# Kernel optimization log

Measured on AMD Instinct MI355X. Metric: run time of the kernel, lower is better.

Reference implementation:

```python
import jax, jax.numpy as jnp
import numpy as np

H = 10  # hidden_dim

def _lstm_layer(x_tbd, w_ih, w_hh, b_ih, b_hh):
    # x_tbd: [T, B, D]; w_ih: [4H, D]; w_hh: [4H, H]; biases [4H]
    B = x_tbd.shape[1]
    h0 = jnp.zeros((B, H), x_tbd.dtype)
    c0 = jnp.zeros((B, H), x_tbd.dtype)
    # precompute input projections for all timesteps: [T, B, 4H]
    xg = jnp.einsum('tbd,gd->tbg', x_tbd, w_ih) + b_ih + b_hh

    def step(carry, xg_t):
        h, c = carry
        gates = xg_t + h @ w_hh.T  # [B, 4H]
        i, f, g, o = jnp.split(gates, 4, axis=-1)  # torch gate order i,f,g,o
        i = jax.nn.sigmoid(i); f = jax.nn.sigmoid(f)
        g = jnp.tanh(g); o = jax.nn.sigmoid(o)
        c = f * c + i * g
        h = o * jnp.tanh(c)
        return (h, c), h

    (hT, cT), hs = jax.lax.scan(step, (h0, c0), xg)
    return hs, hT  # hs: [T, B, H]

def setup_inputs() -> dict:
    key = jax.random.key(0)
    ks = jax.random.split(key, 11)
    B, T, D = 32768, 28, 28
    s0 = 1.0 / np.sqrt(H)
    u = lambda k, shape: jax.random.uniform(k, shape, jnp.float32, -s0, s0)
    return {
        'x': jax.random.normal(ks[0], (B, T, D), jnp.float32),
        'w_ih0': u(ks[1], (4 * H, D)),
        'w_hh0': u(ks[2], (4 * H, H)),
        'b_ih0': u(ks[3], (4 * H,)),
        'b_hh0': u(ks[4], (4 * H,)),
        'w_ih1': u(ks[5], (4 * H, H)),
        'w_hh1': u(ks[6], (4 * H, H)),
        'b_ih1': u(ks[7], (4 * H,)),
        'b_hh1': u(ks[8], (4 * H,)),
        'w_cls': u(ks[9], (10, H)),
        'b_cls': u(ks[10], (10,)),
    }

def reference(x, w_ih0, w_hh0, b_ih0, b_hh0, w_ih1, w_hh1, b_ih1, b_hh1, w_cls, b_cls):
    x_tbd = jnp.swapaxes(x, 0, 1)  # [T, B, D]
    hs0, _ = _lstm_layer(x_tbd, w_ih0, w_hh0, b_ih0, b_hh0)
    _, hT1 = _lstm_layer(hs0, w_ih1, w_hh1, b_ih1, b_hh1)  # hT1 = h_n[-1]
    return hT1 @ w_cls.T + b_cls  # [B, 10]
```

## Files before the change

### kernel.cpp

```cpp
#include <hip/hip_runtime.h>


#define HDIM 10
#define DDIM 28
#define TSTEPS 28

typedef __attribute__((ext_vector_type(8))) short short8;
typedef __attribute__((ext_vector_type(4))) float f32x4;

__device__ __forceinline__ unsigned short bf16_rne(float f) {
    unsigned u = __builtin_bit_cast(unsigned, f);
    u += 0x7FFFu + ((u >> 16) & 1u);
    return (unsigned short)(u >> 16);
}
__device__ __forceinline__ float bf16_f(unsigned short h) {
    unsigned u = ((unsigned)h) << 16;
    return __builtin_bit_cast(float, u);
}
__device__ __forceinline__ unsigned pk_hl(float v) {
    unsigned a, p;
    const float z = 0.0f;
    asm("v_cvt_pk_bf16_f32 %0, %1, %2" : "=v"(a) : "v"(v), "v"(z));
    const float hif = __builtin_bit_cast(float, a << 16);
    const float d = v - hif;
    asm("v_cvt_pk_bf16_f32 %0, %1, %2" : "=v"(p) : "v"(v), "v"(d));
    return p;
}
__device__ __forceinline__ float sig_f(float v) {
    return __builtin_amdgcn_rcpf(1.0f + __expf(-v));
}
__device__ __forceinline__ float tanh_f(float v) {
    return 2.0f * __builtin_amdgcn_rcpf(1.0f + __expf(-2.0f * v)) - 1.0f;
}

#define FENCE() __asm volatile("" ::: "memory")
#define WR32(arrp, sidx, val) (*(unsigned*)&(arrp)[(sidx)] = (val))

__global__ __launch_bounds__(64) void lstm2_mfma_kernel(
    const float* __restrict__ x,
    const float* __restrict__ w_ih0, const float* __restrict__ w_hh0,
    const float* __restrict__ b_ih0, const float* __restrict__ b_hh0,
    const float* __restrict__ w_ih1, const float* __restrict__ w_hh1,
    const float* __restrict__ b_ih1, const float* __restrict__ b_hh1,
    const float* __restrict__ w_cls, const float* __restrict__ b_cls,
    float* __restrict__ out)
{
    __shared__ unsigned short uA0[16 * 136];
    __shared__ unsigned short uA1[16 * 72];
    __shared__ float hfin[16 * 12];

    const int l  = threadIdx.x;
    const int lm = l & 15;
    const int q  = l >> 4;
    const int sbase = blockIdx.x * 16;

    for (int i = l; i < 16 * 22; i += 64) uA0[(i / 22) * 136 + 114 + (i % 22)] = 0;
    for (int i = l; i < 16 * 12; i += 64) uA1[(i / 12) * 72 + 60 + (i % 12)] = 0;

    short8 B0[4][4], B1[4][2];
    const bool gvalid = (lm < 10);
    #pragma unroll
    for (int T = 0; T < 4; ++T) {
        const int g = 10 * T + lm;
        #pragma unroll
        for (int c = 0; c < 4; ++c) {
            #pragma unroll
            for (int j = 0; j < 8; ++j) {
                const int kk = 32 * c + 8 * q + j;
                unsigned short bits = 0;
                if (gvalid && kk < 114) {
                    if (kk < 76) {
                        const int j2 = kk >> 1;
                        const float w = (j2 < 28) ? w_ih0[g * 28 + j2]
                                                  : w_hh0[g * 10 + (j2 - 28)];
                        bits = bf16_rne(w);
                    } else {
                        const int d = kk - 76;
                        const float w = (d < 28) ? w_ih0[g * 28 + d]
                                                 : w_hh0[g * 10 + (d - 28)];
                        const unsigned short hi = bf16_rne(w);
                        bits = bf16_rne(w - bf16_f(hi));
                    }
                }
                B0[T][c][j] = (short)bits;
            }
        }
        #pragma unroll
        for (int c = 0; c < 2; ++c) {
            #pragma unroll
            for (int j = 0; j < 8; ++j) {
                const int kk = 32 * c + 8 * q + j;
                unsigned short bits = 0;
                if (gvalid && kk < 60) {
                    if (kk < 40) {
                        const int j2 = kk >> 1;
                        const float w = (j2 < 10) ? w_ih1[g * 10 + j2]
                                                  : w_hh1[g * 10 + (j2 - 10)];
                        bits = bf16_rne(w);
                    } else {
                        const int d = kk - 40;
                        const float w = (d < 10) ? w_ih1[g * 10 + d]
                                                 : w_hh1[g * 10 + (d - 10)];
                        const unsigned short hi = bf16_rne(w);
                        bits = bf16_rne(w - bf16_f(hi));
                    }
                }
                B1[T][c][j] = (short)bits;
            }
        }
    }

    float bias0[4], bias1[4];
    #pragma unroll
    for (int T = 0; T < 4; ++T) {
        const int g = 10 * T + lm;
        bias0[T] = gvalid ? (b_ih0[g] + b_hh0[g]) : 0.0f;
        bias1[T] = gvalid ? (b_ih1[g] + b_hh1[g]) : 0.0f;
    }

    int xoff[7], lofsA[7], lofsB[7]; float xn[7];
    #pragma unroll
    for (int i = 0; i < 7; ++i) {
        const int f = l + 64 * i;
        const int sm = f / 28, d = f - 28 * sm;
        lofsA[i] = sm * 136 + 2 * d;
        lofsB[i] = sm * 136 + 76 + d;
        xoff[i] = (sbase + sm) * (TSTEPS * DDIM) + d;
        xn[i] = x[xoff[i]];
    }
    #pragma unroll
    for (int i = 0; i < 7; ++i) {
        const unsigned p = pk_hl(xn[i]);
        WR32(uA0, lofsA[i], p);
        uA0[lofsB[i]] = (unsigned short)p;
    }
    if (lm < 10) {
        #pragma unroll
        for (int r = 0; r < 4; ++r) {
            const int m = 4 * q + r;
            unsigned short* r0 = &uA0[m * 136];
            WR32(r0, 56 + 2 * lm, 0u); r0[104 + lm] = 0;
            unsigned short* r1 = &uA1[m * 72];
            WR32(r1, 2 * lm, 0u);      r1[40 + lm] = 0;
            WR32(r1, 20 + 2 * lm, 0u); r1[50 + lm] = 0;
        }
    }
    FENCE();

    float c0s[4] = {0, 0, 0, 0}, c1s[4] = {0, 0, 0, 0};
    float h1v[4] = {0, 0, 0, 0};
    float h0v[4];
    short8 A0f[4], A1f[2];

    #pragma unroll
    for (int c = 0; c < 4; ++c)
        A0f[c] = *(const short8*)&uA0[lm * 136 + 32 * c + 8 * q];
    FENCE();
    #pragma unroll
    for (int i = 0; i < 7; ++i) { xoff[i] += DDIM; xn[i] = x[xoff[i]]; }
    {
        f32x4 C[4];
        #pragma unroll
        for (int T = 0; T < 4; ++T) {
            f32x4 acc = {bias0[T], bias0[T], bias0[T], bias0[T]};
            #pragma unroll
            for (int c = 0; c < 4; ++c)
                acc = __builtin_amdgcn_mfma_f32_16x16x32_bf16(A0f[c], B0[T][c], acc, 0, 0, 0);
            C[T] = acc;
        }
        #pragma unroll
        for (int r = 0; r < 4; ++r) {
            const float i0 = sig_f(C[0][r]);
            const float f0 = sig_f(C[1][r]);
            const float g0 = tanh_f(C[2][r]);
            const float o0 = sig_f(C[3][r]);
            const float c0 = f0 * c0s[r] + i0 * g0;
            c0s[r] = c0;
            h0v[r] = o0 * tanh_f(c0);
        }
        if (lm < 10) {
            #pragma unroll
            for (int r = 0; r < 4; ++r) {
                const int m = 4 * q + r;
                const unsigned p0 = pk_hl(h0v[r]);
                unsigned short* r0 = &uA0[m * 136];
                WR32(r0, 56 + 2 * lm, p0); r0[104 + lm] = (unsigned short)p0;
                unsigned short* r1 = &uA1[m * 72];
                WR32(r1, 2 * lm, p0);      r1[40 + lm] = (unsigned short)p0;
            }
        }
        #pragma unroll
        for (int i = 0; i < 7; ++i) {
            const unsigned p = pk_hl(xn[i]);
            WR32(uA0, lofsA[i], p);
            uA0[lofsB[i]] = (unsigned short)p;
        }
    }
    FENCE();

    #pragma unroll 1
    for (int t = 0; t < TSTEPS - 1; ++t) {
        #pragma unroll
        for (int c = 0; c < 2; ++c)
            A1f[c] = *(const short8*)&uA1[lm * 72 + 32 * c + 8 * q];
        #pragma unroll
        for (int c = 0; c < 4; ++c)
            A0f[c] = *(const short8*)&uA0[lm * 136 + 32 * c + 8 * q];
        FENCE();

        if (t < TSTEPS - 2) {
            #pragma unroll
            for (int i = 0; i < 7; ++i) { xoff[i] += DDIM; xn[i] = x[xoff[i]]; }
        }

        f32x4 C[4], D[4];
        #pragma unroll
        for (int T = 0; T < 4; ++T) {
            f32x4 accD = {bias1[T], bias1[T], bias1[T], bias1[T]};
            #pragma unroll
            for (int c = 0; c < 2; ++c)
                accD = __builtin_amdgcn_mfma_f32_16x16x32_bf16(A1f[c], B1[T][c], accD, 0, 0, 0);
            D[T] = accD;
            f32x4 accC = {bias0[T], bias0[T], bias0[T], bias0[T]};
            #pragma unroll
            for (int c = 0; c < 4; ++c)
                accC = __builtin_amdgcn_mfma_f32_16x16x32_bf16(A0f[c], B0[T][c], accC, 0, 0, 0);
            C[T] = accC;
        }

        #pragma unroll
        for (int r = 0; r < 4; ++r) {
            const float i1 = sig_f(D[0][r]);
            const float f1 = sig_f(D[1][r]);
            const float g1 = tanh_f(D[2][r]);
            const float o1 = sig_f(D[3][r]);
            const float c1 = f1 * c1s[r] + i1 * g1;
            c1s[r] = c1;
            h1v[r] = o1 * tanh_f(c1);
            const float i0 = sig_f(C[0][r]);
            const float f0 = sig_f(C[1][r]);
            const float g0 = tanh_f(C[2][r]);
            const float o0 = sig_f(C[3][r]);
            const float c0 = f0 * c0s[r] + i0 * g0;
            c0s[r] = c0;
            h0v[r] = o0 * tanh_f(c0);
        }

        if (lm < 10) {
            #pragma unroll
            for (int r = 0; r < 4; ++r) {
                const int m = 4 * q + r;
                const unsigned p1 = pk_hl(h1v[r]);
                unsigned short* r1 = &uA1[m * 72];
                WR32(r1, 20 + 2 * lm, p1); r1[50 + lm] = (unsigned short)p1;
                const unsigned p0 = pk_hl(h0v[r]);
                WR32(r1, 2 * lm, p0);      r1[40 + lm] = (unsigned short)p0;
                unsigned short* r0 = &uA0[m * 136];
                WR32(r0, 56 + 2 * lm, p0); r0[104 + lm] = (unsigned short)p0;
            }
        }
        if (t < TSTEPS - 2) {
            #pragma unroll
            for (int i = 0; i < 7; ++i) {
                const unsigned p = pk_hl(xn[i]);
                WR32(uA0, lofsA[i], p);
                uA0[lofsB[i]] = (unsigned short)p;
            }
        }
        FENCE();
    }

    {
        #pragma unroll
        for (int c = 0; c < 2; ++c)
            A1f[c] = *(const short8*)&uA1[lm * 72 + 32 * c + 8 * q];
        FENCE();
        f32x4 D[4];
        #pragma unroll
        for (int T = 0; T < 4; ++T) {
            f32x4 acc = {bias1[T], bias1[T], bias1[T], bias1[T]};
            #pragma unroll
            for (int c = 0; c < 2; ++c)
                acc = __builtin_amdgcn_mfma_f32_16x16x32_bf16(A1f[c], B1[T][c], acc, 0, 0, 0);
            D[T] = acc;
        }
        #pragma unroll
        for (int r = 0; r < 4; ++r) {
            const float i1 = sig_f(D[0][r]);
            const float f1 = sig_f(D[1][r]);
            const float g1 = tanh_f(D[2][r]);
            const float o1 = sig_f(D[3][r]);
            const float c1 = f1 * c1s[r] + i1 * g1;
            h1v[r] = o1 * tanh_f(c1);
        }
    }

    if (lm < 10) {
        #pragma unroll
        for (int r = 0; r < 4; ++r) hfin[(4 * q + r) * 12 + lm] = h1v[r];
    }
    FENCE();
    if (lm < 10) {
        float wc[10];
        #pragma unroll
        for (int j = 0; j < 10; ++j) wc[j] = w_cls[lm * 10 + j];
        const float bo = b_cls[lm];
        #pragma unroll
        for (int r = 0; r < 4; ++r) {
            const int m = 4 * q + r;
            float acc = bo;
            #pragma unroll
            for (int j = 0; j < 10; ++j) acc += hfin[m * 12 + j] * wc[j];
            out[(size_t)(sbase + m) * 10 + lm] = acc;
        }
    }
}

extern "C" void kernel_launch(void* const* d_in, const int* in_sizes, int n_in,
                              void* d_out, int out_size, void* d_ws, size_t ws_size,
                              hipStream_t stream) {
    const float* x     = (const float*)d_in[0];
    const float* w_ih0 = (const float*)d_in[1];
    const float* w_hh0 = (const float*)d_in[2];
    const float* b_ih0 = (const float*)d_in[3];
    const float* b_hh0 = (const float*)d_in[4];
    const float* w_ih1 = (const float*)d_in[5];
    const float* w_hh1 = (const float*)d_in[6];
    const float* b_ih1 = (const float*)d_in[7];
    const float* b_hh1 = (const float*)d_in[8];
    const float* w_cls = (const float*)d_in[9];
    const float* b_cls = (const float*)d_in[10];
    float* out = (float*)d_out;

    const int B = in_sizes[0] / (TSTEPS * DDIM);
    const int grid = B / 16;

    hipLaunchKernelGGL(lstm2_mfma_kernel, dim3(grid), dim3(64), 0, stream,
                       x, w_ih0, w_hh0, b_ih0, b_hh0,
                       w_ih1, w_hh1, b_ih1, b_hh1,
                       w_cls, b_cls, out);
}
```

Measured before the change: 268.4 us.

## Pack four independent waves per block and double-buffer x prefetch two steps ahead

Each block now holds four waves, each running its own 16-sample LSTM tile with private LDS slices, which cuts the grid size by four. The timestep loop is unrolled by two and alternates between two register buffers for x, so the global load for step t+2 is issued while step t is computed. This is meant to hide global-load latency on the serial recurrence and lower per-block launch overhead. The cost is more registers per thread, which may lower occupancy.

```diff
diff --git a/kernel.cpp b/kernel.cpp
--- a/kernel.cpp
+++ b/kernel.cpp
@@ -36,7 +36,74 @@
 #define FENCE() __asm volatile("" ::: "memory")
 #define WR32(arrp, sidx, val) (*(unsigned*)&(arrp)[(sidx)] = (val))
 
-__global__ __launch_bounds__(64) void lstm2_mfma_kernel(
+#define BODY(P, Q, T) do {                                                    \
+    _Pragma("unroll")                                                         \
+    for (int c = 0; c < 2; ++c)                                               \
+        A1f[c] = *(const short8*)&uA1w[lm * 72 + 32 * c + 8 * q];             \
+    _Pragma("unroll")                                                         \
+    for (int c = 0; c < 4; ++c)                                               \
+        A0f[c] = *(const short8*)&uA0w[lm * 136 + 32 * c + 8 * q];            \
+    FENCE();                                                                  \
+    if ((T) < TSTEPS - 3) {                                                   \
+        _Pragma("unroll")                                                     \
+        for (int i = 0; i < 7; ++i) { xoff[i] += DDIM; Q[i] = x[xoff[i]]; }   \
+    }                                                                         \
+    f32x4 C[4], D[4];                                                         \
+    _Pragma("unroll")                                                         \
+    for (int T4 = 0; T4 < 4; ++T4) {                                          \
+        f32x4 accD = {bias1[T4], bias1[T4], bias1[T4], bias1[T4]};            \
+        _Pragma("unroll")                                                     \
+        for (int c = 0; c < 2; ++c)                                           \
+            accD = __builtin_amdgcn_mfma_f32_16x16x32_bf16(A1f[c], B1[T4][c], accD, 0, 0, 0); \
+        D[T4] = accD;                                                         \
+        f32x4 accC = {bias0[T4], bias0[T4], bias0[T4], bias0[T4]};            \
+        _Pragma("unroll")                                                     \
+        for (int c = 0; c < 4; ++c)                                           \
+            accC = __builtin_amdgcn_mfma_f32_16x16x32_bf16(A0f[c], B0[T4][c], accC, 0, 0, 0); \
+        C[T4] = accC;                                                         \
+    }                                                                         \
+    _Pragma("unroll")                                                         \
+    for (int r = 0; r < 4; ++r) {                                             \
+        const float i1 = sig_f(D[0][r]);                                      \
+        const float f1 = sig_f(D[1][r]);                                      \
+        const float g1 = tanh_f(D[2][r]);                                     \
+        const float o1 = sig_f(D[3][r]);                                      \
+        const float c1 = f1 * c1s[r] + i1 * g1;                               \
+        c1s[r] = c1;                                                          \
+        h1v[r] = o1 * tanh_f(c1);                                             \
+        const float i0 = sig_f(C[0][r]);                                      \
+        const float f0 = sig_f(C[1][r]);                                      \
+        const float g0 = tanh_f(C[2][r]);                                     \
+        const float o0 = sig_f(C[3][r]);                                      \
+        const float c0 = f0 * c0s[r] + i0 * g0;                               \
+        c0s[r] = c0;                                                          \
+        h0v[r] = o0 * tanh_f(c0);                                             \
+    }                                                                         \
+    if ((T) < TSTEPS - 2) {                                                   \
+        _Pragma("unroll")                                                     \
+        for (int i = 0; i < 7; ++i) {                                         \
+            const unsigned p = pk_hl(P[i]);                                   \
+            WR32(uA0w, lofsA[i], p);                                          \
+            uA0w[lofsB[i]] = (unsigned short)p;                               \
+        }                                                                     \
+    }                                                                         \
+    if (lm < 10) {                                                            \
+        _Pragma("unroll")                                                     \
+        for (int r = 0; r < 4; ++r) {                                         \
+            const int m = 4 * q + r;                                          \
+            const unsigned p1 = pk_hl(h1v[r]);                                \
+            unsigned short* r1 = &uA1w[m * 72];                               \
+            WR32(r1, 20 + 2 * lm, p1); r1[50 + lm] = (unsigned short)p1;      \
+            const unsigned p0 = pk_hl(h0v[r]);                                \
+            WR32(r1, 2 * lm, p0);      r1[40 + lm] = (unsigned short)p0;      \
+            unsigned short* r0 = &uA0w[m * 136];                              \
+            WR32(r0, 56 + 2 * lm, p0); r0[104 + lm] = (unsigned short)p0;     \
+        }                                                                     \
+    }                                                                         \
+    FENCE();                                                                  \
+} while (0)
+
+__global__ __launch_bounds__(256) void lstm2_mfma_kernel(
     const float* __restrict__ x,
     const float* __restrict__ w_ih0, const float* __restrict__ w_hh0,
     const float* __restrict__ b_ih0, const float* __restrict__ b_hh0,
@@ -45,17 +112,22 @@
     const float* __restrict__ w_cls, const float* __restrict__ b_cls,
     float* __restrict__ out)
 {
-    __shared__ unsigned short uA0[16 * 136];
-    __shared__ unsigned short uA1[16 * 72];
-    __shared__ float hfin[16 * 12];
-
-    const int l  = threadIdx.x;
-    const int lm = l & 15;
-    const int q  = l >> 4;
-    const int sbase = blockIdx.x * 16;
-
-    for (int i = l; i < 16 * 22; i += 64) uA0[(i / 22) * 136 + 114 + (i % 22)] = 0;
-    for (int i = l; i < 16 * 12; i += 64) uA1[(i / 12) * 72 + 60 + (i % 12)] = 0;
+    __shared__ __align__(16) unsigned short uA0s[4][16 * 136];
+    __shared__ __align__(16) unsigned short uA1s[4][16 * 72];
+    __shared__ __align__(16) float hfins[4][16 * 12];
+
+    const int l   = threadIdx.x & 63;
+    const int wid = threadIdx.x >> 6;
+    const int lm  = l & 15;
+    const int q   = l >> 4;
+    const int sbase = (blockIdx.x * 4 + wid) * 16;
+
+    unsigned short* const uA0w = uA0s[wid];
+    unsigned short* const uA1w = uA1s[wid];
+    float* const hfinw = hfins[wid];
+
+    for (int i = l; i < 16 * 22; i += 64) uA0w[(i / 22) * 136 + 114 + (i % 22)] = 0;
+    for (int i = l; i < 16 * 12; i += 64) uA1w[(i / 12) * 72 + 60 + (i % 12)] = 0;
 
     short8 B0[4][4], B1[4][2];
     const bool gvalid = (lm < 10);
@@ -118,7 +190,8 @@
         bias1[T] = gvalid ? (b_ih1[g] + b_hh1[g]) : 0.0f;
     }
 
-    int xoff[7], lofsA[7], lofsB[7]; float xn[7];
+    int xoff[7], lofsA[7], lofsB[7];
+    float xA[7], xB[7];
     #pragma unroll
     for (int i = 0; i < 7; ++i) {
         const int f = l + 64 * i;
@@ -126,21 +199,21 @@
         lofsA[i] = sm * 136 + 2 * d;
         lofsB[i] = sm * 136 + 76 + d;
         xoff[i] = (sbase + sm) * (TSTEPS * DDIM) + d;
-        xn[i] = x[xoff[i]];
+        xA[i] = x[xoff[i]];
     }
     #pragma unroll
     for (int i = 0; i < 7; ++i) {
-        const unsigned p = pk_hl(xn[i]);
-        WR32(uA0, lofsA[i], p);
-        uA0[lofsB[i]] = (unsigned short)p;
+        const unsigned p = pk_hl(xA[i]);
+        WR32(uA0w, lofsA[i], p);
+        uA0w[lofsB[i]] = (unsigned short)p;
     }
     if (lm < 10) {
         #pragma unroll
         for (int r = 0; r < 4; ++r) {
             const int m = 4 * q + r;
-            unsigned short* r0 = &uA0[m * 136];
+            unsigned short* r0 = &uA0w[m * 136];
             WR32(r0, 56 + 2 * lm, 0u); r0[104 + lm] = 0;
-            unsigned short* r1 = &uA1[m * 72];
+            unsigned short* r1 = &uA1w[m * 72];
             WR32(r1, 2 * lm, 0u);      r1[40 + lm] = 0;
             WR32(r1, 20 + 2 * lm, 0u); r1[50 + lm] = 0;
         }
@@ -153,11 +226,14 @@
     short8 A0f[4], A1f[2];
 
     #pragma unroll
+    for (int i = 0; i < 7; ++i) { xoff[i] += DDIM; xA[i] = x[xoff[i]]; }
+
+    #pragma unroll
     for (int c = 0; c < 4; ++c)
-        A0f[c] = *(const short8*)&uA0[lm * 136 + 32 * c + 8 * q];
+        A0f[c] = *(const short8*)&uA0w[lm * 136 + 32 * c + 8 * q];
     FENCE();
     #pragma unroll
-    for (int i = 0; i < 7; ++i) { xoff[i] += DDIM; xn[i] = x[xoff[i]]; }
+    for (int i = 0; i < 7; ++i) { xoff[i] += DDIM; xB[i] = x[xoff[i]]; }
     {
         f32x4 C[4];
         #pragma unroll
@@ -183,97 +259,32 @@
             for (int r = 0; r < 4; ++r) {
                 const int m = 4 * q + r;
                 const unsigned p0 = pk_hl(h0v[r]);
-                unsigned short* r0 = &uA0[m * 136];
+                unsigned short* r0 = &uA0w[m * 136];
                 WR32(r0, 56 + 2 * lm, p0); r0[104 + lm] = (unsigned short)p0;
-                unsigned short* r1 = &uA1[m * 72];
+                unsigned short* r1 = &uA1w[m * 72];
                 WR32(r1, 2 * lm, p0);      r1[40 + lm] = (unsigned short)p0;
             }
         }
         #pragma unroll
         for (int i = 0; i < 7; ++i) {
-            const unsigned p = pk_hl(xn[i]);
-            WR32(uA0, lofsA[i], p);
-            uA0[lofsB[i]] = (unsigned short)p;
+            const unsigned p = pk_hl(xA[i]);
+            WR32(uA0w, lofsA[i], p);
+            uA0w[lofsB[i]] = (unsigned short)p;
         }
     }
     FENCE();
 
     #pragma unroll 1
-    for (int t = 0; t < TSTEPS - 1; ++t) {
+    for (int tp = 0; tp < 13; ++tp) {
+        BODY(xB, xA, 2 * tp);
+        BODY(xA, xB, 2 * tp + 1);
+    }
+    BODY(xB, xA, 26);
+
+    {
         #pragma unroll
         for (int c = 0; c < 2; ++c)
-            A1f[c] = *(const short8*)&uA1[lm * 72 + 32 * c + 8 * q];
-        #pragma unroll
-        for (int c = 0; c < 4; ++c)
-            A0f[c] = *(const short8*)&uA0[lm * 136 + 32 * c + 8 * q];
-        FENCE();
-
-        if (t < TSTEPS - 2) {
-            #pragma unroll
-            for (int i = 0; i < 7; ++i) { xoff[i] += DDIM; xn[i] = x[xoff[i]]; }
-        }
-
-        f32x4 C[4], D[4];
-        #pragma unroll
-        for (int T = 0; T < 4; ++T) {
-            f32x4 accD = {bias1[T], bias1[T], bias1[T], bias1[T]};
-            #pragma unroll
-            for (int c = 0; c < 2; ++c)
-                accD = __builtin_amdgcn_mfma_f32_16x16x32_bf16(A1f[c], B1[T][c], accD, 0, 0, 0);
-            D[T] = accD;
-            f32x4 accC = {bias0[T], bias0[T], bias0[T], bias0[T]};
-            #pragma unroll
-            for (int c = 0; c < 4; ++c)
-                accC = __builtin_amdgcn_mfma_f32_16x16x32_bf16(A0f[c], B0[T][c], accC, 0, 0, 0);
-            C[T] = accC;
-        }
-
-        #pragma unroll
-        for (int r = 0; r < 4; ++r) {
-            const float i1 = sig_f(D[0][r]);
-            const float f1 = sig_f(D[1][r]);
-            const float g1 = tanh_f(D[2][r]);
-            const float o1 = sig_f(D[3][r]);
-            const float c1 = f1 * c1s[r] + i1 * g1;
-            c1s[r] = c1;
-            h1v[r] = o1 * tanh_f(c1);
-            const float i0 = sig_f(C[0][r]);
-            const float f0 = sig_f(C[1][r]);
-            const float g0 = tanh_f(C[2][r]);
-            const float o0 = sig_f(C[3][r]);
-            const float c0 = f0 * c0s[r] + i0 * g0;
-            c0s[r] = c0;
-            h0v[r] = o0 * tanh_f(c0);
-        }
-
-        if (lm < 10) {
-            #pragma unroll
-            for (int r = 0; r < 4; ++r) {
-                const int m = 4 * q + r;
-                const unsigned p1 = pk_hl(h1v[r]);
-                unsigned short* r1 = &uA1[m * 72];
-                WR32(r1, 20 + 2 * lm, p1); r1[50 + lm] = (unsigned short)p1;
-                const unsigned p0 = pk_hl(h0v[r]);
-                WR32(r1, 2 * lm, p0);      r1[40 + lm] = (unsigned short)p0;
-                unsigned short* r0 = &uA0[m * 136];
-                WR32(r0, 56 + 2 * lm, p0); r0[104 + lm] = (unsigned short)p0;
-            }
-        }
-        if (t < TSTEPS - 2) {
-            #pragma unroll
-            for (int i = 0; i < 7; ++i) {
-                const unsigned p = pk_hl(xn[i]);
-                WR32(uA0, lofsA[i], p);
-                uA0[lofsB[i]] = (unsigned short)p;
-            }
-        }
-        FENCE();
-    }
-
-    {
-        #pragma unroll
-        for (int c = 0; c < 2; ++c)
-            A1f[c] = *(const short8*)&uA1[lm * 72 + 32 * c + 8 * q];
+            A1f[c] = *(const short8*)&uA1w[lm * 72 + 32 * c + 8 * q];
         FENCE();
         f32x4 D[4];
         #pragma unroll
@@ -297,7 +308,7 @@
 
     if (lm < 10) {
         #pragma unroll
-        for (int r = 0; r < 4; ++r) hfin[(4 * q + r) * 12 + lm] = h1v[r];
+        for (int r = 0; r < 4; ++r) hfinw[(4 * q + r) * 12 + lm] = h1v[r];
     }
     FENCE();
     if (lm < 10) {
@@ -310,7 +321,7 @@
             const int m = 4 * q + r;
             float acc = bo;
             #pragma unroll
-            for (int j = 0; j < 10; ++j) acc += hfin[m * 12 + j] * wc[j];
+            for (int j = 0; j < 10; ++j) acc += hfinw[m * 12 + j] * wc[j];
             out[(size_t)(sbase + m) * 10 + lm] = acc;
         }
     }
@@ -333,9 +344,9 @@
     float* out = (float*)d_out;
 
     const int B = in_sizes[0] / (TSTEPS * DDIM);
-    const int grid = B / 16;
-
-    hipLaunchKernelGGL(lstm2_mfma_kernel, dim3(grid), dim3(64), 0, stream,
+    const int grid = B / 64;
+
+    hipLaunchKernelGGL(lstm2_mfma_kernel, dim3(grid), dim3(256), 0, stream,
                        x, w_ih0, w_hh0, b_ih0, b_hh0,
                        w_ih1, w_hh1, b_ih1, b_hh1,
                        w_cls, b_cls, out);
```

Measured after the change: 265.8 us. About the same (-1.0%).
